# Performance work log

Hardware: AMD Instinct MI355X
Metric: run time of the kernel (lower is better)

The kernel has to match this reference:

```python
import jax, jax.numpy as jnp
import numpy as np

D = 1024
H = 16
DK = D // H
TB = 64  # temporal_bias_dim
SCALE = DK ** -0.5


def setup_inputs() -> dict:
    key = jax.random.key(0)
    ks = jax.random.split(key, 12)
    B, S = 8, 512
    s = 0.02
    return {
        "x": jax.random.normal(ks[0], (B, S, D), jnp.float32),
        "padding_masks": jnp.ones((B, 1, 1, S), jnp.int32),
        "batch_temporal_mat": jax.random.uniform(ks[1], (B, S, S), jnp.float32) * 100.0,
        "wq": jax.random.normal(ks[2], (D, D), jnp.float32) * s,
        "bq": jnp.zeros((D,), jnp.float32),
        "wk": jax.random.normal(ks[3], (D, D), jnp.float32) * s,
        "bk": jnp.zeros((D,), jnp.float32),
        "wv": jax.random.normal(ks[4], (D, D), jnp.float32) * s,
        "bv": jnp.zeros((D,), jnp.float32),
        "w_proj": jax.random.normal(ks[5], (D, D), jnp.float32) * s,
        "b_proj": jnp.zeros((D,), jnp.float32),
        "w_tb1": jax.random.normal(ks[6], (1, TB), jnp.float32) * 0.5,
        "b_tb1": jnp.zeros((TB,), jnp.float32),
        "w_tb2": jax.random.normal(ks[7], (TB, 1), jnp.float32) * 0.5,
        "b_tb2": jnp.zeros((1,), jnp.float32),
    }


def reference(x, padding_masks, batch_temporal_mat, wq, bq, wk, bk, wv, bv,
              w_proj, b_proj, w_tb1, b_tb1, w_tb2, b_tb2):
    B, S, _ = x.shape

    def heads(w, b):
        return (x @ w + b).reshape(B, S, H, DK).transpose(0, 2, 1, 3)  # (B,H,S,DK)

    q, k, v = heads(wq, bq), heads(wk, bk), heads(wv, bv)
    scores = jnp.einsum("bhqd,bhkd->bhqk", q, k) * SCALE  # (B,H,S,S)

    # temporal bias: 1/log(e + t) -> Linear(1,64) -> leaky_relu(0.2) -> Linear(64,1)
    t = 1.0 / jnp.log(jnp.exp(jnp.float32(1.0)) + batch_temporal_mat)  # (B,S,S)
    h = t[..., None] * w_tb1[0] + b_tb1  # (B,S,S,TB)
    h = jnp.where(h >= 0, h, 0.2 * h)
    bias = (h @ w_tb2)[..., 0] + b_tb2[0]  # (B,S,S)
    scores = scores + bias[:, None, :, :]

    neg_inf = jnp.float32(-jnp.inf)
    scores = jnp.where(padding_masks == 0, neg_inf, scores)
    causal = jnp.triu(jnp.ones((S, S), bool), k=1)  # (S,S), add_cls=False
    scores = jnp.where(causal[None, None], neg_inf, scores)

    p_attn = jax.nn.softmax(scores, axis=-1)
    out = jnp.einsum("bhqk,bhkd->bhqd", p_attn, v)
    out = out.transpose(0, 2, 1, 3).reshape(B, S, D)
    out = out @ w_proj + b_proj
    return out
```

## Files before the change

kernel.cpp:

```cpp
#include <hip/hip_runtime.h>
#include <hip/hip_bf16.h>

#define B_  8
#define S_  512
#define D_  1024
#define H_  16
#define DK_ 64
#define TB_ 64
#define SCALE_ 0.125f

typedef __attribute__((ext_vector_type(8))) short          bh8;
typedef __attribute__((ext_vector_type(4))) float          f32x4;
typedef __attribute__((ext_vector_type(8))) unsigned short us8;

__device__ __forceinline__ unsigned short f2bf(float f) {
    unsigned u = __float_as_uint(f);
    unsigned r = 0x7fffu + ((u >> 16) & 1u);
    return (unsigned short)((u + r) >> 16);
}

__global__ __launch_bounds__(256)
void cvt_x_kernel(const float* __restrict__ in, unsigned short* __restrict__ out, int n8)
{
    int i = blockIdx.x * 256 + threadIdx.x;
    if (i >= n8) return;
    float4 a = *(const float4*)&in[(size_t)i * 8];
    float4 b = *(const float4*)&in[(size_t)i * 8 + 4];
    us8 o;
    o[0] = f2bf(a.x); o[1] = f2bf(a.y); o[2] = f2bf(a.z); o[3] = f2bf(a.w);
    o[4] = f2bf(b.x); o[5] = f2bf(b.y); o[6] = f2bf(b.z); o[7] = f2bf(b.w);
    *(us8*)&out[(size_t)i * 8] = o;
}

__global__ __launch_bounds__(256)
void cvt_wt_kernel(const float* __restrict__ W, unsigned short* __restrict__ Wt)
{
    __shared__ float t[64][65];
    const int bx = blockIdx.x, by = blockIdx.y;
    const int c  = threadIdx.x & 63;
    const int r0 = threadIdx.x >> 6;
    #pragma unroll
    for (int i = 0; i < 16; ++i) {
        int r = r0 + i * 4;
        t[r][c] = W[(size_t)(by * 64 + r) * 1024 + bx * 64 + c];
    }
    __syncthreads();
    #pragma unroll
    for (int i = 0; i < 16; ++i) {
        int r = r0 + i * 4;
        Wt[(size_t)(bx * 64 + r) * 1024 + by * 64 + c] = f2bf(t[c][r]);
    }
}

__global__ __launch_bounds__(256)
void gemm_qkv_kernel(const unsigned short* __restrict__ A,
                     const unsigned short* __restrict__ Wt,
                     const float* __restrict__ bq, const float* __restrict__ bk,
                     const float* __restrict__ bv,
                     unsigned short* __restrict__ qo,
                     unsigned short* __restrict__ ko,
                     unsigned short* __restrict__ vo)
{
    __shared__ unsigned short As[128][72];
    __shared__ unsigned short Bs[64][72];
    const int tid  = threadIdx.x;
    const int lane = tid & 63;
    const int wid  = tid >> 6;
    const int wr   = wid >> 1, wc = wid & 1;
    const int row0 = blockIdx.x * 128;
    const int col0 = blockIdx.y * 64;

    f32x4 acc[4][2] = {};

    const int ur = tid >> 3;
    const int uc = (tid & 7) * 8;
    const int fr = lane & 15;
    const int fk = (lane >> 4) * 8;
    const int g  = lane >> 4;

    for (int k0 = 0; k0 < 1024; k0 += 64) {
        __syncthreads();
        #pragma unroll
        for (int i = 0; i < 4; ++i) {
            int r = ur + i * 32;
            *(int4*)&As[r][uc] = *(const int4*)&A[(size_t)(row0 + r) * 1024 + k0 + uc];
        }
        #pragma unroll
        for (int i = 0; i < 2; ++i) {
            int r = ur + i * 32;
            *(int4*)&Bs[r][uc] = *(const int4*)&Wt[(size_t)(col0 + r) * 1024 + k0 + uc];
        }
        __syncthreads();
        #pragma unroll
        for (int ks = 0; ks < 2; ++ks) {
            bh8 af[4], bfr[2];
            #pragma unroll
            for (int r = 0; r < 4; ++r)
                af[r]  = *(const bh8*)&As[wr * 64 + r * 16 + fr][ks * 32 + fk];
            #pragma unroll
            for (int c = 0; c < 2; ++c)
                bfr[c] = *(const bh8*)&Bs[wc * 32 + c * 16 + fr][ks * 32 + fk];
            #pragma unroll
            for (int r = 0; r < 4; ++r)
                #pragma unroll
                for (int c = 0; c < 2; ++c)
                    acc[r][c] = __builtin_amdgcn_mfma_f32_16x16x32_bf16(
                        af[r], bfr[c], acc[r][c], 0, 0, 0);
        }
    }

    const int nh = col0 >> 10;
    const float* bsel = (nh == 0) ? bq : (nh == 1) ? bk : bv;
    unsigned short* outp = (nh == 0) ? qo : (nh == 1) ? ko : vo;

    #pragma unroll
    for (int r = 0; r < 4; ++r) {
        #pragma unroll
        for (int c = 0; c < 2; ++c) {
            int n  = col0 + wc * 32 + c * 16 + (lane & 15);
            int nn = n & 1023;
            float bn = bsel[nn];
            int hh = nn >> 6, dd = nn & 63;
            #pragma unroll
            for (int j = 0; j < 4; ++j) {
                int m = row0 + wr * 64 + r * 16 + g * 4 + j;
                float o = acc[r][c][j] + bn;
                int bb = m >> 9, ss = m & 511;
                if (nh == 2)
                    outp[((size_t)((bb * H_ + hh) * DK_ + dd)) * S_ + ss] = f2bf(o);
                else
                    outp[((size_t)((bb * H_ + hh) * S_ + ss)) * DK_ + dd] = f2bf(o);
            }
        }
    }
}

__global__ __launch_bounds__(256)
void gemm_proj_kernel(const unsigned short* __restrict__ A,
                      const unsigned short* __restrict__ Wt,
                      const float* __restrict__ bias,
                      float* __restrict__ C)
{
    __shared__ unsigned short As[128][72];
    __shared__ unsigned short Bs[64][72];
    const int tid  = threadIdx.x;
    const int lane = tid & 63;
    const int wid  = tid >> 6;
    const int wr   = wid >> 1, wc = wid & 1;
    const int row0 = blockIdx.x * 128;
    const int col0 = blockIdx.y * 64;

    f32x4 acc[4][2] = {};

    const int ur = tid >> 3;
    const int uc = (tid & 7) * 8;
    const int fr = lane & 15;
    const int fk = (lane >> 4) * 8;
    const int g  = lane >> 4;

    for (int k0 = 0; k0 < 1024; k0 += 64) {
        __syncthreads();
        #pragma unroll
        for (int i = 0; i < 4; ++i) {
            int r = ur + i * 32;
            *(int4*)&As[r][uc] = *(const int4*)&A[(size_t)(row0 + r) * 1024 + k0 + uc];
        }
        #pragma unroll
        for (int i = 0; i < 2; ++i) {
            int r = ur + i * 32;
            *(int4*)&Bs[r][uc] = *(const int4*)&Wt[(size_t)(col0 + r) * 1024 + k0 + uc];
        }
        __syncthreads();
        #pragma unroll
        for (int ks = 0; ks < 2; ++ks) {
            bh8 af[4], bfr[2];
            #pragma unroll
            for (int r = 0; r < 4; ++r)
                af[r]  = *(const bh8*)&As[wr * 64 + r * 16 + fr][ks * 32 + fk];
            #pragma unroll
            for (int c = 0; c < 2; ++c)
                bfr[c] = *(const bh8*)&Bs[wc * 32 + c * 16 + fr][ks * 32 + fk];
            #pragma unroll
            for (int r = 0; r < 4; ++r)
                #pragma unroll
                for (int c = 0; c < 2; ++c)
                    acc[r][c] = __builtin_amdgcn_mfma_f32_16x16x32_bf16(
                        af[r], bfr[c], acc[r][c], 0, 0, 0);
        }
    }

    #pragma unroll
    for (int r = 0; r < 4; ++r) {
        #pragma unroll
        for (int c = 0; c < 2; ++c) {
            int n = col0 + wc * 32 + c * 16 + (lane & 15);
            float bn = bias[n];
            #pragma unroll
            for (int j = 0; j < 4; ++j) {
                int m = row0 + wr * 64 + r * 16 + g * 4 + j;
                C[(size_t)m * 1024 + n] = acc[r][c][j] + bn;
            }
        }
    }
}

__global__ __launch_bounds__(256)
void tbias_kernel(const float* __restrict__ tm, const int* __restrict__ pmask,
                  const float* __restrict__ w1, const float* __restrict__ b1,
                  const float* __restrict__ w2, const float* __restrict__ b2,
                  float* __restrict__ bias)
{
    __shared__ float sw1[TB_], sb1[TB_], sw2[TB_];
    if (threadIdx.x < TB_) {
        sw1[threadIdx.x] = w1[threadIdx.x];
        sb1[threadIdx.x] = b1[threadIdx.x];
        sw2[threadIdx.x] = w2[threadIdx.x];
    }
    __syncthreads();
    const float ec  = 2.7182818284590452f;
    const float b2v = b2[0];
    const int n = B_ * S_ * S_;
    for (int i = blockIdx.x * blockDim.x + threadIdx.x; i < n;
         i += gridDim.x * blockDim.x) {
        int bb = i >> 18;
        int jj = i & (S_ - 1);
        float t   = 1.0f / logf(ec + tm[i]);
        float acc = b2v;
        #pragma unroll
        for (int j = 0; j < TB_; ++j) {
            float h = fmaf(t, sw1[j], sb1[j]);
            h = (h >= 0.f) ? h : 0.2f * h;
            acc = fmaf(h, sw2[j], acc);
        }
        bias[i] = (pmask[bb * S_ + jj] == 0) ? -1e30f : acc;
    }
}

__global__ __launch_bounds__(256)
void attn_kernel(const unsigned short* __restrict__ q,
                 const unsigned short* __restrict__ k,
                 const unsigned short* __restrict__ vt,
                 const float* __restrict__ biasm,
                 unsigned short* __restrict__ outb)
{
    __shared__ unsigned short Kl[64][72];
    __shared__ unsigned short Vl[64][72];
    __shared__ unsigned short Pl[64][72];

    const int tid  = threadIdx.x;
    const int lane = tid & 63;
    const int w    = tid >> 6;
    const int lin = (blockIdx.x & 7) * 128 + (blockIdx.x >> 3);
    const int h   = lin & 15;
    const int qt  = (lin >> 4) & 7;
    const int b   = lin >> 7;
    const int q0  = qt * 64;

    const int l15 = lane & 15;
    const int g   = lane >> 4;

    const size_t hb  = (size_t)(b * H_ + h) * S_;
    const unsigned short* kbase  = k  + hb * DK_;
    const unsigned short* vtbase = vt + ((size_t)(b * H_ + h) * DK_) * S_;

    const int qrow_a = q0 + w * 16 + l15;
    bh8 aq0 = *(const bh8*)&q[(hb + qrow_a) * DK_ +      g * 8];
    bh8 aq1 = *(const bh8*)&q[(hb + qrow_a) * DK_ + 32 + g * 8];

    const int qd = q0 + w * 16 + g * 4;

    f32x4 acc_o[4] = {};
    float m_run[4] = { -1e30f, -1e30f, -1e30f, -1e30f };
    float l_run[4] = {};

    for (int kt = 0; kt <= qt; ++kt) {
        __syncthreads();
        #pragma unroll
        for (int s = 0; s < 2; ++s) {
            int u  = tid + s * 256;
            int r  = u >> 3;
            int c8 = (u & 7) * 8;
            *(int4*)&Kl[r][c8] = *(const int4*)&kbase [(size_t)(kt * 64 + r) * DK_ + c8];
            *(int4*)&Vl[r][c8] = *(const int4*)&vtbase[(size_t)r * S_ + kt * 64 + c8];
        }
        __syncthreads();

        f32x4 sc[4];
        #pragma unroll
        for (int c = 0; c < 4; ++c) {
            bh8 bk0 = *(const bh8*)&Kl[c * 16 + l15][     g * 8];
            bh8 bk1 = *(const bh8*)&Kl[c * 16 + l15][32 + g * 8];
            f32x4 z = {};
            z = __builtin_amdgcn_mfma_f32_16x16x32_bf16(aq0, bk0, z, 0, 0, 0);
            sc[c] = __builtin_amdgcn_mfma_f32_16x16x32_bf16(aq1, bk1, z, 0, 0, 0);
        }

        float sv[4][4];
        #pragma unroll
        for (int j = 0; j < 4; ++j) {
            const float* br = biasm + ((size_t)b * S_ + qd + j) * S_ + kt * 64;
            #pragma unroll
            for (int c = 0; c < 4; ++c)
                sv[c][j] = fmaf(sc[c][j], SCALE_, br[c * 16 + l15]);
        }
        if (kt == qt) {
            #pragma unroll
            for (int c = 0; c < 4; ++c) {
                int kloc = c * 16 + l15;
                #pragma unroll
                for (int j = 0; j < 4; ++j)
                    if (kloc > w * 16 + g * 4 + j) sv[c][j] = -1e30f;
            }
        }

        #pragma unroll
        for (int j = 0; j < 4; ++j) {
            float mt = fmaxf(fmaxf(sv[0][j], sv[1][j]), fmaxf(sv[2][j], sv[3][j]));
            mt = fmaxf(mt, __shfl_xor(mt, 1));
            mt = fmaxf(mt, __shfl_xor(mt, 2));
            mt = fmaxf(mt, __shfl_xor(mt, 4));
            mt = fmaxf(mt, __shfl_xor(mt, 8));
            float m_new = fmaxf(m_run[j], mt);
            float resc  = __expf(m_run[j] - m_new);
            float psum  = 0.f;
            #pragma unroll
            for (int c = 0; c < 4; ++c) {
                float p = __expf(sv[c][j] - m_new);
                Pl[w * 16 + g * 4 + j][c * 16 + l15] = f2bf(p);
                psum += p;
            }
            psum += __shfl_xor(psum, 1);
            psum += __shfl_xor(psum, 2);
            psum += __shfl_xor(psum, 4);
            psum += __shfl_xor(psum, 8);
            l_run[j] = l_run[j] * resc + psum;
            m_run[j] = m_new;
            acc_o[0][j] *= resc; acc_o[1][j] *= resc;
            acc_o[2][j] *= resc; acc_o[3][j] *= resc;
        }

        asm volatile("s_waitcnt lgkmcnt(0)" ::: "memory");

        bh8 ap0 = *(const bh8*)&Pl[w * 16 + l15][     g * 8];
        bh8 ap1 = *(const bh8*)&Pl[w * 16 + l15][32 + g * 8];
        #pragma unroll
        for (int c2 = 0; c2 < 4; ++c2) {
            bh8 bv0 = *(const bh8*)&Vl[c2 * 16 + l15][     g * 8];
            bh8 bv1 = *(const bh8*)&Vl[c2 * 16 + l15][32 + g * 8];
            acc_o[c2] = __builtin_amdgcn_mfma_f32_16x16x32_bf16(ap0, bv0, acc_o[c2], 0, 0, 0);
            acc_o[c2] = __builtin_amdgcn_mfma_f32_16x16x32_bf16(ap1, bv1, acc_o[c2], 0, 0, 0);
        }
    }

    #pragma unroll
    for (int j = 0; j < 4; ++j) {
        float linv = 1.f / l_run[j];
        #pragma unroll
        for (int c2 = 0; c2 < 4; ++c2)
            outb[((size_t)(b * S_ + qd + j)) * D_ + h * DK_ + c2 * 16 + l15] =
                f2bf(acc_o[c2][j] * linv);
    }
}

extern "C" void kernel_launch(void* const* d_in, const int* in_sizes, int n_in,
                              void* d_out, int out_size, void* d_ws, size_t ws_size,
                              hipStream_t stream)
{
    const float* x     = (const float*)d_in[0];
    const int*   pm    = (const int*)  d_in[1];
    const float* tm    = (const float*)d_in[2];
    const float* wq    = (const float*)d_in[3];
    const float* bq    = (const float*)d_in[4];
    const float* wk    = (const float*)d_in[5];
    const float* bk    = (const float*)d_in[6];
    const float* wv    = (const float*)d_in[7];
    const float* bv    = (const float*)d_in[8];
    const float* wp    = (const float*)d_in[9];
    const float* bp    = (const float*)d_in[10];
    const float* w_tb1 = (const float*)d_in[11];
    const float* b_tb1 = (const float*)d_in[12];
    const float* w_tb2 = (const float*)d_in[13];
    const float* b_tb2 = (const float*)d_in[14];

    char* wsb = (char*)d_ws;
    const size_t MB = 1u << 20;
    unsigned short* xb   = (unsigned short*)wsb;
    unsigned short* wqkv = (unsigned short*)(wsb + 8  * MB);
    unsigned short* wtp  = (unsigned short*)(wsb + 14 * MB);
    unsigned short* qw   = (unsigned short*)(wsb + 16 * MB);
    unsigned short* kw   = (unsigned short*)(wsb + 24 * MB);
    unsigned short* vtw  = (unsigned short*)(wsb + 32 * MB);
    float*          bw   = (float*)        (wsb + 40 * MB);

    cvt_x_kernel<<<2048, 256, 0, stream>>>(x, xb, 524288);
    dim3 gw(16, 16);
    cvt_wt_kernel<<<gw, 256, 0, stream>>>(wq, wqkv);
    cvt_wt_kernel<<<gw, 256, 0, stream>>>(wk, wqkv + 1048576);
    cvt_wt_kernel<<<gw, 256, 0, stream>>>(wv, wqkv + 2097152);
    cvt_wt_kernel<<<gw, 256, 0, stream>>>(wp, wtp);

    dim3 gqkv(32, 48);
    gemm_qkv_kernel<<<gqkv, 256, 0, stream>>>(xb, wqkv, bq, bk, bv, qw, kw, vtw);

    tbias_kernel<<<2048, 256, 0, stream>>>(tm, pm, w_tb1, b_tb1, w_tb2, b_tb2, bw);

    attn_kernel<<<1024, 256, 0, stream>>>(qw, kw, vtw, bw, xb );

    dim3 gp(32, 16);
    gemm_proj_kernel<<<gp, 256, 0, stream>>>(xb, wtp, bp, (float*)d_out);
}
```

Before: 229.1 us.

## Use direct global-to-LDS loads and 128x128 tiles in projection GEMMs

Replaces register-staged global-to-shared copies in the QKV and output projection GEMMs with global_load_lds 16-byte transfers into an unpadded LDS layout. The QKV GEMM tile widens from 128x64 to 128x128, with each wave computing a 64x64 sub-tile, to increase reuse of A and halve the grid. The aim is to cut VGPR traffic and load instructions and to raise arithmetic intensity. The unpadded layout may introduce LDS bank conflicts, and the larger accumulator raises register pressure.

```diff
diff --git a/kernel.cpp b/kernel.cpp
--- a/kernel.cpp
+++ b/kernel.cpp
@@ -17,6 +17,12 @@
     unsigned u = __float_as_uint(f);
     unsigned r = 0x7fffu + ((u >> 16) & 1u);
     return (unsigned short)((u + r) >> 16);
+}
+
+__device__ __forceinline__ void gl16(const unsigned short* g, unsigned short* l) {
+    __builtin_amdgcn_global_load_lds(
+        (const __attribute__((address_space(1))) void*)g,
+        (__attribute__((address_space(3))) void*)l, 16, 0, 0);
 }
 
 __global__ __launch_bounds__(256)
@@ -61,52 +67,49 @@
                      unsigned short* __restrict__ ko,
                      unsigned short* __restrict__ vo)
 {
-    __shared__ unsigned short As[128][72];
-    __shared__ unsigned short Bs[64][72];
+    __shared__ unsigned short As[128 * 64];
+    __shared__ unsigned short Bs[128 * 64];
     const int tid  = threadIdx.x;
     const int lane = tid & 63;
     const int wid  = tid >> 6;
     const int wr   = wid >> 1, wc = wid & 1;
     const int row0 = blockIdx.x * 128;
-    const int col0 = blockIdx.y * 64;
-
-    f32x4 acc[4][2] = {};
-
-    const int ur = tid >> 3;
-    const int uc = (tid & 7) * 8;
-    const int fr = lane & 15;
-    const int fk = (lane >> 4) * 8;
-    const int g  = lane >> 4;
+    const int col0 = blockIdx.y * 128;
+
+    f32x4 acc[4][4] = {};
+
+    const int fr   = lane & 15;
+    const int fk   = (lane >> 4) * 8;
+    const int g    = lane >> 4;
+    const int srow = wid * 32 + (lane >> 3);
+    const int scol = (lane & 7) * 8;
 
     for (int k0 = 0; k0 < 1024; k0 += 64) {
-        __syncthreads();
         #pragma unroll
         for (int i = 0; i < 4; ++i) {
-            int r = ur + i * 32;
-            *(int4*)&As[r][uc] = *(const int4*)&A[(size_t)(row0 + r) * 1024 + k0 + uc];
-        }
-        #pragma unroll
-        for (int i = 0; i < 2; ++i) {
-            int r = ur + i * 32;
-            *(int4*)&Bs[r][uc] = *(const int4*)&Wt[(size_t)(col0 + r) * 1024 + k0 + uc];
+            gl16(&A [(size_t)(row0 + srow + i * 8) * 1024 + k0 + scol],
+                 &As[(wid * 32 + i * 8) * 64]);
+            gl16(&Wt[(size_t)(col0 + srow + i * 8) * 1024 + k0 + scol],
+                 &Bs[(wid * 32 + i * 8) * 64]);
         }
         __syncthreads();
         #pragma unroll
         for (int ks = 0; ks < 2; ++ks) {
-            bh8 af[4], bfr[2];
+            bh8 af[4], bfr[4];
             #pragma unroll
             for (int r = 0; r < 4; ++r)
-                af[r]  = *(const bh8*)&As[wr * 64 + r * 16 + fr][ks * 32 + fk];
-            #pragma unroll
-            for (int c = 0; c < 2; ++c)
-                bfr[c] = *(const bh8*)&Bs[wc * 32 + c * 16 + fr][ks * 32 + fk];
+                af[r]  = *(const bh8*)&As[(wr * 64 + r * 16 + fr) * 64 + ks * 32 + fk];
+            #pragma unroll
+            for (int c = 0; c < 4; ++c)
+                bfr[c] = *(const bh8*)&Bs[(wc * 64 + c * 16 + fr) * 64 + ks * 32 + fk];
             #pragma unroll
             for (int r = 0; r < 4; ++r)
                 #pragma unroll
-                for (int c = 0; c < 2; ++c)
+                for (int c = 0; c < 4; ++c)
                     acc[r][c] = __builtin_amdgcn_mfma_f32_16x16x32_bf16(
                         af[r], bfr[c], acc[r][c], 0, 0, 0);
         }
+        __syncthreads();
     }
 
     const int nh = col0 >> 10;
@@ -116,8 +119,8 @@
     #pragma unroll
     for (int r = 0; r < 4; ++r) {
         #pragma unroll
-        for (int c = 0; c < 2; ++c) {
-            int n  = col0 + wc * 32 + c * 16 + (lane & 15);
+        for (int c = 0; c < 4; ++c) {
+            int n  = col0 + wc * 64 + c * 16 + (lane & 15);
             int nn = n & 1023;
             float bn = bsel[nn];
             int hh = nn >> 6, dd = nn & 63;
@@ -141,8 +144,8 @@
                       const float* __restrict__ bias,
                       float* __restrict__ C)
 {
-    __shared__ unsigned short As[128][72];
-    __shared__ unsigned short Bs[64][72];
+    __shared__ unsigned short As[128 * 64];
+    __shared__ unsigned short Bs[64 * 64];
     const int tid  = threadIdx.x;
     const int lane = tid & 63;
     const int wid  = tid >> 6;
@@ -152,34 +155,32 @@
 
     f32x4 acc[4][2] = {};
 
-    const int ur = tid >> 3;
-    const int uc = (tid & 7) * 8;
-    const int fr = lane & 15;
-    const int fk = (lane >> 4) * 8;
-    const int g  = lane >> 4;
+    const int fr   = lane & 15;
+    const int fk   = (lane >> 4) * 8;
+    const int g    = lane >> 4;
+    const int srow = wid * 32 + (lane >> 3);
+    const int scol = (lane & 7) * 8;
+    const int brow = wid * 16 + (lane >> 3);
 
     for (int k0 = 0; k0 < 1024; k0 += 64) {
-        __syncthreads();
-        #pragma unroll
-        for (int i = 0; i < 4; ++i) {
-            int r = ur + i * 32;
-            *(int4*)&As[r][uc] = *(const int4*)&A[(size_t)(row0 + r) * 1024 + k0 + uc];
-        }
-        #pragma unroll
-        for (int i = 0; i < 2; ++i) {
-            int r = ur + i * 32;
-            *(int4*)&Bs[r][uc] = *(const int4*)&Wt[(size_t)(col0 + r) * 1024 + k0 + uc];
-        }
+        #pragma unroll
+        for (int i = 0; i < 4; ++i)
+            gl16(&A [(size_t)(row0 + srow + i * 8) * 1024 + k0 + scol],
+                 &As[(wid * 32 + i * 8) * 64]);
+        #pragma unroll
+        for (int i = 0; i < 2; ++i)
+            gl16(&Wt[(size_t)(col0 + brow + i * 8) * 1024 + k0 + scol],
+                 &Bs[(wid * 16 + i * 8) * 64]);
         __syncthreads();
         #pragma unroll
         for (int ks = 0; ks < 2; ++ks) {
             bh8 af[4], bfr[2];
             #pragma unroll
             for (int r = 0; r < 4; ++r)
-                af[r]  = *(const bh8*)&As[wr * 64 + r * 16 + fr][ks * 32 + fk];
+                af[r]  = *(const bh8*)&As[(wr * 64 + r * 16 + fr) * 64 + ks * 32 + fk];
             #pragma unroll
             for (int c = 0; c < 2; ++c)
-                bfr[c] = *(const bh8*)&Bs[wc * 32 + c * 16 + fr][ks * 32 + fk];
+                bfr[c] = *(const bh8*)&Bs[(wc * 32 + c * 16 + fr) * 64 + ks * 32 + fk];
             #pragma unroll
             for (int r = 0; r < 4; ++r)
                 #pragma unroll
@@ -187,6 +188,7 @@
                     acc[r][c] = __builtin_amdgcn_mfma_f32_16x16x32_bf16(
                         af[r], bfr[c], acc[r][c], 0, 0, 0);
         }
+        __syncthreads();
     }
 
     #pragma unroll
@@ -399,7 +401,7 @@
     cvt_wt_kernel<<<gw, 256, 0, stream>>>(wv, wqkv + 2097152);
     cvt_wt_kernel<<<gw, 256, 0, stream>>>(wp, wtp);
 
-    dim3 gqkv(32, 48);
+    dim3 gqkv(32, 24);
     gemm_qkv_kernel<<<gqkv, 256, 0, stream>>>(xb, wqkv, bq, bk, bv, qw, kw, vtw);
 
     tbias_kernel<<<2048, 256, 0, stream>>>(tm, pm, w_tb1, b_tb1, w_tb2, b_tb2, bw);
```

After: 248.4 us. 1.08x slower.
